# Kernel tuning notes

Measured on AMD Instinct MI355X. Metric: run time of the kernel, lower is better.

## Reference

```python
import jax, jax.numpy as jnp
import numpy as np

B, S, D, H = 16, 1024, 768, 12
HS = D // H  # head size = 64
NEG = -1000000.0  # module uses -1e6, not -inf


def setup_inputs() -> dict:
    key = jax.random.key(0)
    k1, k2, k3 = jax.random.split(key, 3)
    scale = 1.0 / np.sqrt(D)
    return {
        "x": jax.random.normal(k1, (B, S, D), dtype=jnp.float32),
        "W_qkv": jax.random.normal(k2, (D, 3 * D), dtype=jnp.float32) * scale,
        "b_qkv": jnp.zeros((3 * D,), dtype=jnp.float32),
        "W_o": jax.random.normal(k3, (D, D), dtype=jnp.float32) * scale,
        "b_o": jnp.zeros((D,), dtype=jnp.float32),
    }


def reference(x, W_qkv, b_qkv, W_o, b_o):
    qkv = x @ W_qkv + b_qkv                      # [B,S,3D]
    q, k, v = jnp.split(qkv, 3, axis=-1)         # each [B,S,D]
    q = q.reshape(B, S, H, HS)
    k = k.reshape(B, S, H, HS)
    v = v.reshape(B, S, H, HS)
    scores = jnp.einsum('bqhd,bkhd->bhqk', q, k) / np.sqrt(HS).astype(np.float32)
    causal = jnp.tril(jnp.ones((S, S), dtype=bool))
    scores = jnp.where(causal, scores, jnp.float32(NEG))
    probs = jax.nn.softmax(scores, axis=-1)      # dropout is eval-mode identity
    av = jnp.einsum('bhqk,bkhd->bqhd', probs, v).reshape(B, S, D)
    return av @ W_o + b_o
```

## Files before the change

### kernel.cpp

```cpp
#include <hip/hip_runtime.h>
#include <stdint.h>

typedef unsigned short u16;
typedef __attribute__((ext_vector_type(8))) short bf16x8;
typedef __attribute__((ext_vector_type(8))) u16 u16x8;
typedef __attribute__((ext_vector_type(4))) u16 u16x4;
typedef __attribute__((ext_vector_type(4))) float f32x4;
typedef __attribute__((ext_vector_type(16))) float f32x16;

#define B_ 16
#define S_ 1024
#define D_ 768
#define H_ 12

__device__ __forceinline__ float bf2f(u16 u) {
  unsigned int x = ((unsigned int)u) << 16;
  float f;
  __builtin_memcpy(&f, &x, 4);
  return f;
}
__device__ __forceinline__ u16 f2bf(float f) {
  unsigned int x;
  __builtin_memcpy(&x, &f, 4);
  x += 0x7fffu + ((x >> 16) & 1u);
  return (u16)(x >> 16);
}

#define MFMA16(a, b, c) __builtin_amdgcn_mfma_f32_16x16x32_bf16((a), (b), (c), 0, 0, 0)
#define MFMA32(a, b, c) __builtin_amdgcn_mfma_f32_32x32x16_bf16((a), (b), (c), 0, 0, 0)

#define GLD16(g, l)                                              \
  __builtin_amdgcn_global_load_lds(                              \
      (const __attribute__((address_space(1))) void*)(g),        \
      (__attribute__((address_space(3))) void*)(l), 16, 0, 0)

__global__ __launch_bounds__(256) void cvt_bf16(const float* __restrict__ in,
                                                u16* __restrict__ out, int n8) {
  const int i = blockIdx.x * 256 + threadIdx.x;
  if (i >= n8) return;
  const float4 a = *(const float4*)(in + (size_t)i * 8);
  const float4 b = *(const float4*)(in + (size_t)i * 8 + 4);
  u16x8 o;
  o[0] = f2bf(a.x); o[1] = f2bf(a.y); o[2] = f2bf(a.z); o[3] = f2bf(a.w);
  o[4] = f2bf(b.x); o[5] = f2bf(b.y); o[6] = f2bf(b.z); o[7] = f2bf(b.w);
  *(u16x8*)(out + (size_t)i * 8) = o;
}

__global__ __launch_bounds__(256) void transpose_cvt(const float* __restrict__ W,
                                                     u16* __restrict__ Wt, int K, int N) {
  __shared__ u16 t[32][33];
  const int n0 = blockIdx.x * 32, k0 = blockIdx.y * 32;
  const int tx = threadIdx.x & 31, ty = threadIdx.x >> 5;
#pragma unroll
  for (int i = 0; i < 32; i += 8)
    t[ty + i][tx] = f2bf(W[(size_t)(k0 + ty + i) * N + n0 + tx]);
  __syncthreads();
#pragma unroll
  for (int i = 0; i < 32; i += 8) Wt[(size_t)(n0 + ty + i) * K + k0 + tx] = t[tx][ty + i];
}

template <int MODE>
__global__ __launch_bounds__(256) void gemm_bt(const u16* __restrict__ A,
                                               const u16* __restrict__ Bt,
                                               const float* __restrict__ bias,
                                               u16* __restrict__ O0, u16* __restrict__ O1,
                                               u16* __restrict__ O2, float* __restrict__ Of,
                                               int M, int N, int K) {
  __shared__ u16 Al[128 * 32];
  __shared__ u16 Bl[128 * 32];
  const int tid = threadIdx.x;
  const int wid = tid >> 6, lane = tid & 63;
  const int lo = lane & 15, hi = lane >> 4;
  const int wr = wid >> 1, wc = wid & 1;
  const int m0 = blockIdx.x * 128, n0 = blockIdx.y * 128;
  const int rA = lane >> 2;
  const int kc = (lane & 3) * 8;
  f32x4 acc[4][4] = {};
  const int kiters = K >> 5;
  for (int kt = 0; kt < kiters; ++kt) {
    const int k0 = kt * 32;
    __syncthreads();
#pragma unroll
    for (int ld = 0; ld < 2; ++ld) {
      const int row = ld * 64 + wid * 16 + rA;
      const int boff = ld * 4096 + wid * 1024;
      GLD16(A + (size_t)(m0 + row) * K + k0 + kc, (char*)Al + boff);
      GLD16(Bt + (size_t)(n0 + row) * K + k0 + kc, (char*)Bl + boff);
    }
    __syncthreads();
    bf16x8 af[4], bfr[4];
#pragma unroll
    for (int i = 0; i < 4; ++i)
      af[i] = *(const bf16x8*)&Al[(wr * 64 + i * 16 + lo) * 32 + hi * 8];
#pragma unroll
    for (int j = 0; j < 4; ++j)
      bfr[j] = *(const bf16x8*)&Bl[(wc * 64 + j * 16 + lo) * 32 + hi * 8];
#pragma unroll
    for (int i = 0; i < 4; ++i)
#pragma unroll
      for (int j = 0; j < 4; ++j) acc[i][j] = MFMA16(af[i], bfr[j], acc[i][j]);
  }
#pragma unroll
  for (int j = 0; j < 4; ++j) {
    const int n = n0 + wc * 64 + j * 16 + lo;
    const float bv = bias[n];
#pragma unroll
    for (int i = 0; i < 4; ++i) {
#pragma unroll
      for (int r = 0; r < 4; ++r) {
        const int m = m0 + wr * 64 + i * 16 + hi * 4 + r;
        const float fv = acc[i][j][r] + bv;
        if (MODE == 0) {
          const u16 o = f2bf(fv);
          if (n0 < D_) {
            O0[(size_t)m * D_ + n] = o;
          } else if (n0 < 2 * D_) {
            O1[(size_t)m * D_ + (n - D_)] = o;
          } else {
            const int np = n - 2 * D_;
            O2[(((size_t)(m >> 10) * H_ + (np >> 6)) * 64 + (np & 63)) * S_ + (m & 1023)] = o;
          }
        } else {
          Of[(size_t)m * N + n] = fv;
        }
      }
    }
  }
}

__global__ __launch_bounds__(256) void attn_fwd2(const u16* __restrict__ Qb,
                                                 const u16* __restrict__ Kb,
                                                 const u16* __restrict__ VTb,
                                                 u16* __restrict__ att) {
  __shared__ u16 Kl[2048];
  __shared__ u16 Vl[2048];
  const int tid = threadIdx.x;
  const int lane = tid & 63, wid = tid >> 6;
  const int l31 = lane & 31, hi1 = lane >> 5;
  const int L = blockIdx.x + 8 * (blockIdx.y + 12 * blockIdx.z);
  const int bx = (L >> 3) & 7;
  const int P = (L & 7) + 8 * (L >> 6);
  const int h = P % 12, b = P / 12;
  const int q0 = bx * 128;
  const int qw0 = q0 + wid * 32;
  const int qg = qw0 + l31;
  const size_t rowbase = (size_t)b * S_;

  bf16x8 qf[4];
  {
    const u16* qp = Qb + (rowbase + qg) * D_ + h * 64 + hi1 * 8;
#pragma unroll
    for (int c = 0; c < 4; ++c) {
      bf16x8 v = *(const bf16x8*)(qp + c * 16);
#pragma unroll
      for (int j = 0; j < 8; ++j) v[j] = (short)f2bf(bf2f((u16)v[j]) * 0.125f);
      qf[c] = v;
    }
  }
  float mrun = -3.0e38f, lrun = 0.0f;
  f32x16 o0 = {}, o1 = {};

  const u16* kgp =
      Kb + (rowbase + (tid & 31)) * D_ + h * 64 + (tid >> 6) * 16 + ((tid >> 5) & 1) * 8;
  const u16* vgp = VTb +
                   (((size_t)b * H_ + h) * 64 + ((tid >> 6) & 1) * 32 + (tid & 31)) * S_ +
                   (tid >> 7) * 16 + ((tid >> 5) & 1) * 8;
  char* kdst = (char*)Kl + wid * 1024;
  char* vdst = (char*)Vl + wid * 1024;
  const char* kbase = (const char*)Kl + lane * 16;
  const char* vbase = (const char*)Vl + lane * 16;

  const int kvend = q0 + 128;
  for (int kv0 = 0; kv0 < kvend; kv0 += 32) {
    __syncthreads();
    GLD16(kgp + (size_t)kv0 * D_, kdst);
    GLD16(vgp + kv0, vdst);
    __syncthreads();
    if (kv0 > qw0 + 31) continue;

    f32x16 s = {};
#pragma unroll
    for (int c = 0; c < 4; ++c) s = MFMA32(*(const bf16x8*)(kbase + c * 1024), qf[c], s);

    if (kv0 + 31 > qw0) {
#pragma unroll
      for (int r = 0; r < 16; ++r) {
        const int kvg = kv0 + (r & 3) + 8 * (r >> 2) + 4 * hi1;
        if (kvg > qg) s[r] = -1.0e30f;
      }
    }
    float rm = s[0];
#pragma unroll
    for (int r = 1; r < 16; ++r) rm = fmaxf(rm, s[r]);
    rm = fmaxf(rm, __shfl_xor(rm, 32));
    const float mn = fmaxf(mrun, rm);
    const float fr = __expf(mrun - mn);
    mrun = mn;
    float p[16];
    float rs = 0.0f;
#pragma unroll
    for (int r = 0; r < 16; ++r) {
      p[r] = __expf(s[r] - mn);
      rs += p[r];
    }
    rs += __shfl_xor(rs, 32);
    lrun = lrun * fr + rs;
#pragma unroll
    for (int r = 0; r < 16; ++r) {
      o0[r] *= fr;
      o1[r] *= fr;
    }
    unsigned int pa[4], pb[4];
#pragma unroll
    for (int g = 0; g < 4; ++g) {
      pa[g] = (unsigned)f2bf(p[4 * g]) | ((unsigned)f2bf(p[4 * g + 1]) << 16);
      pb[g] = (unsigned)f2bf(p[4 * g + 2]) | ((unsigned)f2bf(p[4 * g + 3]) << 16);
    }
    const unsigned sa = __shfl_xor(hi1 ? pa[0] : pa[1], 32);
    const unsigned sb = __shfl_xor(hi1 ? pb[0] : pb[1], 32);
    const unsigned sc = __shfl_xor(hi1 ? pa[2] : pa[3], 32);
    const unsigned sd = __shfl_xor(hi1 ? pb[2] : pb[3], 32);
    const uint4 w0 = hi1 ? make_uint4(sa, sb, pa[1], pb[1]) : make_uint4(pa[0], pb[0], sa, sb);
    const uint4 w1 = hi1 ? make_uint4(sc, sd, pa[3], pb[3]) : make_uint4(pa[2], pb[2], sc, sd);
    bf16x8 pf0, pf1;
    __builtin_memcpy(&pf0, &w0, 16);
    __builtin_memcpy(&pf1, &w1, 16);
    o0 = MFMA32(*(const bf16x8*)(vbase + 0 * 1024), pf0, o0);
    o1 = MFMA32(*(const bf16x8*)(vbase + 1 * 1024), pf0, o1);
    o0 = MFMA32(*(const bf16x8*)(vbase + 2 * 1024), pf1, o0);
    o1 = MFMA32(*(const bf16x8*)(vbase + 3 * 1024), pf1, o1);
  }
  const float inv = 1.0f / lrun;
  u16* op = att + (rowbase + qg) * D_ + h * 64;
#pragma unroll
  for (int g = 0; g < 4; ++g) {
    u16x4 v0, v1;
#pragma unroll
    for (int j = 0; j < 4; ++j) {
      v0[j] = f2bf(o0[4 * g + j] * inv);
      v1[j] = f2bf(o1[4 * g + j] * inv);
    }
    *(u16x4*)(op + 8 * g + 4 * hi1) = v0;
    *(u16x4*)(op + 32 + 8 * g + 4 * hi1) = v1;
  }
}

extern "C" void kernel_launch(void* const* d_in, const int* in_sizes, int n_in, void* d_out,
                              int out_size, void* d_ws, size_t ws_size, hipStream_t stream) {
  const float *x = nullptr, *Wqkv = nullptr, *bqkv = nullptr, *Wo = nullptr, *bo = nullptr;
  for (int i = 0; i < n_in; ++i) {
    switch (in_sizes[i]) {
      case 16384 * 768:  x = (const float*)d_in[i]; break;
      case 768 * 2304:   Wqkv = (const float*)d_in[i]; break;
      case 2304:         bqkv = (const float*)d_in[i]; break;
      case 768 * 768:    Wo = (const float*)d_in[i]; break;
      case 768:          bo = (const float*)d_in[i]; break;
    }
  }
  float* out = (float*)d_out;

  char* ws = (char*)d_ws;
  u16* WqkvT = (u16*)(ws);
  u16* WoT = (u16*)(ws + 3538944);
  u16* Qb = (u16*)(ws + 4718592);
  u16* Kb = (u16*)(ws + 29884416);
  u16* VT = (u16*)(ws + 55050240);
  u16* xb = (u16*)d_out;
  u16* att = Qb;

  cvt_bf16<<<(16384 * 768 / 8 + 255) / 256, 256, 0, stream>>>(x, xb, 16384 * 768 / 8);
  transpose_cvt<<<dim3(2304 / 32, 768 / 32), 256, 0, stream>>>(Wqkv, WqkvT, 768, 2304);
  transpose_cvt<<<dim3(768 / 32, 768 / 32), 256, 0, stream>>>(Wo, WoT, 768, 768);
  gemm_bt<0><<<dim3(16384 / 128, 2304 / 128), 256, 0, stream>>>(
      xb, WqkvT, bqkv, Qb, Kb, VT, nullptr, 16384, 2304, 768);
  attn_fwd2<<<dim3(8, H_, B_), 256, 0, stream>>>(Qb, Kb, VT, att);
  gemm_bt<1><<<dim3(16384 / 128, 768 / 128), 256, 0, stream>>>(
      att, WoT, bo, nullptr, nullptr, nullptr, out, 16384, 768, 768);
}
```

Before: 257.4 us.

## Double-buffer GEMM shared-memory tiles to overlap global loads with MFMA

Doubles the LDS A/B tile buffers and prefetches the next K-slice directly into the alternate buffer, issued before the MFMAs on the current buffer. This replaces the two __syncthreads per iteration with a single vmcnt wait plus barrier, so global load latency can hide behind compute. It also raises wave priority around the MFMA block. The cost is doubled LDS per block, which may lower occupancy, and the wait is still a full vmcnt(0) at the end of each iteration.

```diff
diff --git a/kernel.cpp b/kernel.cpp
--- a/kernel.cpp
+++ b/kernel.cpp
@@ -66,8 +66,8 @@
                                                u16* __restrict__ O0, u16* __restrict__ O1,
                                                u16* __restrict__ O2, float* __restrict__ Of,
                                                int M, int N, int K) {
-  __shared__ u16 Al[128 * 32];
-  __shared__ u16 Bl[128 * 32];
+  __shared__ u16 Al[2 * 128 * 32];
+  __shared__ u16 Bl[2 * 128 * 32];
   const int tid = threadIdx.x;
   const int wid = tid >> 6, lane = tid & 63;
   const int lo = lane & 15, hi = lane >> 4;
@@ -75,30 +75,44 @@
   const int m0 = blockIdx.x * 128, n0 = blockIdx.y * 128;
   const int rA = lane >> 2;
   const int kc = (lane & 3) * 8;
+  const int srow = wid * 16 + rA;
   f32x4 acc[4][4] = {};
   const int kiters = K >> 5;
+
+  GLD16(A + (size_t)(m0 + srow) * K + kc, (char*)Al + wid * 1024);
+  GLD16(A + (size_t)(m0 + srow + 64) * K + kc, (char*)Al + 4096 + wid * 1024);
+  GLD16(Bt + (size_t)(n0 + srow) * K + kc, (char*)Bl + wid * 1024);
+  GLD16(Bt + (size_t)(n0 + srow + 64) * K + kc, (char*)Bl + 4096 + wid * 1024);
+  asm volatile("s_waitcnt vmcnt(0)" ::: "memory");
+  __builtin_amdgcn_s_barrier();
+
+  int cur = 0;
   for (int kt = 0; kt < kiters; ++kt) {
-    const int k0 = kt * 32;
-    __syncthreads();
-#pragma unroll
-    for (int ld = 0; ld < 2; ++ld) {
-      const int row = ld * 64 + wid * 16 + rA;
-      const int boff = ld * 4096 + wid * 1024;
-      GLD16(A + (size_t)(m0 + row) * K + k0 + kc, (char*)Al + boff);
-      GLD16(Bt + (size_t)(n0 + row) * K + k0 + kc, (char*)Bl + boff);
-    }
-    __syncthreads();
+    if (kt + 1 < kiters) {
+      const int k0 = (kt + 1) * 32;
+      const int nb = (cur ^ 1) * 8192;
+      GLD16(A + (size_t)(m0 + srow) * K + k0 + kc, (char*)Al + nb + wid * 1024);
+      GLD16(A + (size_t)(m0 + srow + 64) * K + k0 + kc, (char*)Al + nb + 4096 + wid * 1024);
+      GLD16(Bt + (size_t)(n0 + srow) * K + k0 + kc, (char*)Bl + nb + wid * 1024);
+      GLD16(Bt + (size_t)(n0 + srow + 64) * K + k0 + kc, (char*)Bl + nb + 4096 + wid * 1024);
+    }
+    const int cb = cur * 4096;
     bf16x8 af[4], bfr[4];
 #pragma unroll
     for (int i = 0; i < 4; ++i)
-      af[i] = *(const bf16x8*)&Al[(wr * 64 + i * 16 + lo) * 32 + hi * 8];
+      af[i] = *(const bf16x8*)&Al[cb + (wr * 64 + i * 16 + lo) * 32 + hi * 8];
 #pragma unroll
     for (int j = 0; j < 4; ++j)
-      bfr[j] = *(const bf16x8*)&Bl[(wc * 64 + j * 16 + lo) * 32 + hi * 8];
+      bfr[j] = *(const bf16x8*)&Bl[cb + (wc * 64 + j * 16 + lo) * 32 + hi * 8];
+    __builtin_amdgcn_s_setprio(1);
 #pragma unroll
     for (int i = 0; i < 4; ++i)
 #pragma unroll
       for (int j = 0; j < 4; ++j) acc[i][j] = MFMA16(af[i], bfr[j], acc[i][j]);
+    __builtin_amdgcn_s_setprio(0);
+    asm volatile("s_waitcnt vmcnt(0)" ::: "memory");
+    __builtin_amdgcn_s_barrier();
+    cur ^= 1;
   }
 #pragma unroll
   for (int j = 0; j < 4; ++j) {
```

New measurement: 251.9 us. -2.2%, faster.

## Replace GEMM with 256x256-tile double-buffered pipelined kernel and block swizzle

Applied to the files above, without the earlier changes.

Replaces the 128x128 single-buffered GEMM with a 512-thread kernel that computes 256x256 output tiles with K-step 64. LDS is double-buffered and global-to-LDS loads are interleaved between the quadrants of MFMA work, using explicit barriers, waitcnt and setprio. Block indices are swizzled so neighbouring workgroups share operand tiles in cache. The goal is to raise MFMA utilisation and data reuse for the QKV and output projections, at the cost of 128KB of LDS per block, more register pressure, and fewer blocks (192) for the output GEMM.

```diff
diff --git a/kernel.cpp b/kernel.cpp
--- a/kernel.cpp
+++ b/kernel.cpp
@@ -33,6 +33,9 @@
   __builtin_amdgcn_global_load_lds(                              \
       (const __attribute__((address_space(1))) void*)(g),        \
       (__attribute__((address_space(3))) void*)(l), 16, 0, 0)
+
+#define BAR() asm volatile("s_barrier" ::: "memory")
+#define LGKM0() asm volatile("s_waitcnt lgkmcnt(0)" ::: "memory")
 
 __global__ __launch_bounds__(256) void cvt_bf16(const float* __restrict__ in,
                                                 u16* __restrict__ out, int n8) {
@@ -60,56 +63,143 @@
 }
 
 template <int MODE>
-__global__ __launch_bounds__(256) void gemm_bt(const u16* __restrict__ A,
-                                               const u16* __restrict__ Bt,
-                                               const float* __restrict__ bias,
-                                               u16* __restrict__ O0, u16* __restrict__ O1,
-                                               u16* __restrict__ O2, float* __restrict__ Of,
-                                               int M, int N, int K) {
-  __shared__ u16 Al[128 * 32];
-  __shared__ u16 Bl[128 * 32];
+__global__ __launch_bounds__(512, 2) void gemm256(const u16* __restrict__ A,
+                                                  const u16* __restrict__ Bt,
+                                                  const float* __restrict__ bias,
+                                                  u16* __restrict__ O0, u16* __restrict__ O1,
+                                                  u16* __restrict__ O2, float* __restrict__ Of,
+                                                  int M, int N, int K) {
+  __shared__ u16 Ls[65536];
+  char* const ldsA = (char*)Ls;
+  char* const ldsB = (char*)Ls + 65536;
   const int tid = threadIdx.x;
   const int wid = tid >> 6, lane = tid & 63;
   const int lo = lane & 15, hi = lane >> 4;
-  const int wr = wid >> 1, wc = wid & 1;
-  const int m0 = blockIdx.x * 128, n0 = blockIdx.y * 128;
-  const int rA = lane >> 2;
-  const int kc = (lane & 3) * 8;
-  f32x4 acc[4][4] = {};
-  const int kiters = K >> 5;
-  for (int kt = 0; kt < kiters; ++kt) {
-    const int k0 = kt * 32;
-    __syncthreads();
-#pragma unroll
-    for (int ld = 0; ld < 2; ++ld) {
-      const int row = ld * 64 + wid * 16 + rA;
-      const int boff = ld * 4096 + wid * 1024;
-      GLD16(A + (size_t)(m0 + row) * K + k0 + kc, (char*)Al + boff);
-      GLD16(Bt + (size_t)(n0 + row) * K + k0 + kc, (char*)Bl + boff);
-    }
-    __syncthreads();
-    bf16x8 af[4], bfr[4];
-#pragma unroll
-    for (int i = 0; i < 4; ++i)
-      af[i] = *(const bf16x8*)&Al[(wr * 64 + i * 16 + lo) * 32 + hi * 8];
-#pragma unroll
-    for (int j = 0; j < 4; ++j)
-      bfr[j] = *(const bf16x8*)&Bl[(wc * 64 + j * 16 + lo) * 32 + hi * 8];
-#pragma unroll
-    for (int i = 0; i < 4; ++i)
-#pragma unroll
-      for (int j = 0; j < 4; ++j) acc[i][j] = MFMA16(af[i], bfr[j], acc[i][j]);
-  }
-#pragma unroll
-  for (int j = 0; j < 4; ++j) {
-    const int n = n0 + wc * 64 + j * 16 + lo;
+  const int wr = wid >> 2, wc = wid & 3;
+  const int nwg = gridDim.x;
+  const int swz = (blockIdx.x & 7) * (nwg >> 3) + (blockIdx.x >> 3);
+  const int nbm = M >> 8;
+  const int mb = swz % nbm, nb = swz / nbm;
+  const int m0 = mb * 256, n0 = nb * 256;
+
+  const u16* const srcA = A + (size_t)(m0 + lo) * K + hi * 8;
+  const u16* const srcB = Bt + (size_t)(n0 + lo) * K + hi * 8;
+  const size_t aoff = (size_t)(wid >> 1) * 16 * K + (wid & 1) * 32;
+
+#define STG_A(ha, kt, bb)                                                        \
+  do {                                                                           \
+    GLD16(srcA + (size_t)(ha) * 128 * K + aoff + (size_t)(kt) * 64,              \
+          ldsA + (bb) * 32768 + (ha) * 16384 + wid * 1024);                      \
+    GLD16(srcA + (size_t)(ha) * 128 * K + aoff + (size_t)64 * K + (size_t)(kt) * 64, \
+          ldsA + (bb) * 32768 + (ha) * 16384 + 8192 + wid * 1024);               \
+  } while (0)
+#define STG_B(hb, kt, bb)                                                        \
+  do {                                                                           \
+    GLD16(srcB + (size_t)(hb) * 128 * K + aoff + (size_t)(kt) * 64,              \
+          ldsB + (bb) * 32768 + (hb) * 16384 + wid * 1024);                      \
+    GLD16(srcB + (size_t)(hb) * 128 * K + aoff + (size_t)64 * K + (size_t)(kt) * 64, \
+          ldsB + (bb) * 32768 + (hb) * 16384 + 8192 + wid * 1024);               \
+  } while (0)
+
+  const char* const rdA = ldsA + wr * 16384 + lane * 16;
+  const char* const rdB = ldsB + (wc >> 1) * 16384 + (wc & 1) * 8192 + lane * 16;
+
+  f32x4 acc[8][4] = {};
+  const int T = K >> 6;
+
+  STG_A(0, 0, 0); STG_A(1, 0, 0); STG_B(0, 0, 0); STG_B(1, 0, 0);
+  STG_B(0, 1, 1); STG_A(0, 1, 1);
+  asm volatile("s_waitcnt vmcnt(4)" ::: "memory");
+  BAR();
+
+  for (int t = 0; t < T; ++t) {
+    const int curb = t & 1, nxtb = curb ^ 1;
+    const int cur = curb * 32768;
+    const bool s1 = (t + 1 < T), s2 = (t + 2 < T);
+    bf16x8 af[4][2], ah[4][2], bl[2][2], bh[2][2];
+#pragma unroll
+    for (int f = 0; f < 4; ++f)
+#pragma unroll
+      for (int s = 0; s < 2; ++s)
+        af[f][s] = *(const bf16x8*)(rdA + cur + (f * 2 + s) * 1024);
+#pragma unroll
+    for (int g = 0; g < 2; ++g)
+#pragma unroll
+      for (int s = 0; s < 2; ++s)
+        bl[g][s] = *(const bf16x8*)(rdB + cur + (g * 2 + s) * 1024);
+    if (s1) STG_A(1, t + 1, nxtb);
+    BAR(); LGKM0();
+    __builtin_amdgcn_s_setprio(1);
+#pragma unroll
+    for (int f = 0; f < 4; ++f)
+#pragma unroll
+      for (int g = 0; g < 2; ++g)
+#pragma unroll
+        for (int s = 0; s < 2; ++s) acc[f][g] = MFMA16(af[f][s], bl[g][s], acc[f][g]);
+    __builtin_amdgcn_s_setprio(0);
+    BAR();
+#pragma unroll
+    for (int g = 0; g < 2; ++g)
+#pragma unroll
+      for (int s = 0; s < 2; ++s)
+        bh[g][s] = *(const bf16x8*)(rdB + cur + ((2 + g) * 2 + s) * 1024);
+    if (s1) STG_B(1, t + 1, nxtb);
+    BAR(); LGKM0();
+    __builtin_amdgcn_s_setprio(1);
+#pragma unroll
+    for (int f = 0; f < 4; ++f)
+#pragma unroll
+      for (int g = 0; g < 2; ++g)
+#pragma unroll
+        for (int s = 0; s < 2; ++s) acc[f][2 + g] = MFMA16(af[f][s], bh[g][s], acc[f][2 + g]);
+    __builtin_amdgcn_s_setprio(0);
+    BAR();
+#pragma unroll
+    for (int f = 0; f < 4; ++f)
+#pragma unroll
+      for (int s = 0; s < 2; ++s)
+        ah[f][s] = *(const bf16x8*)(rdA + cur + ((4 + f) * 2 + s) * 1024);
+    if (s2) STG_B(0, t + 2, curb);
+    BAR(); LGKM0();
+    __builtin_amdgcn_s_setprio(1);
+#pragma unroll
+    for (int f = 0; f < 4; ++f)
+#pragma unroll
+      for (int g = 0; g < 2; ++g)
+#pragma unroll
+        for (int s = 0; s < 2; ++s)
+          acc[4 + f][2 + g] = MFMA16(ah[f][s], bh[g][s], acc[4 + f][2 + g]);
+    __builtin_amdgcn_s_setprio(0);
+    BAR();
+    if (s2) STG_A(0, t + 2, curb);
+    BAR();
+    __builtin_amdgcn_s_setprio(1);
+#pragma unroll
+    for (int f = 0; f < 4; ++f)
+#pragma unroll
+      for (int g = 0; g < 2; ++g)
+#pragma unroll
+        for (int s = 0; s < 2; ++s) acc[4 + f][g] = MFMA16(ah[f][s], bl[g][s], acc[4 + f][g]);
+    __builtin_amdgcn_s_setprio(0);
+    if (s2) {
+      asm volatile("s_waitcnt vmcnt(4)" ::: "memory");
+    } else if (s1) {
+      asm volatile("s_waitcnt vmcnt(0)" ::: "memory");
+    }
+    BAR();
+  }
+#undef STG_A
+#undef STG_B
+#pragma unroll
+  for (int g = 0; g < 4; ++g) {
+    const int n = n0 + wc * 64 + g * 16 + lo;
     const float bv = bias[n];
 #pragma unroll
-    for (int i = 0; i < 4; ++i) {
+    for (int f = 0; f < 8; ++f) {
 #pragma unroll
       for (int r = 0; r < 4; ++r) {
-        const int m = m0 + wr * 64 + i * 16 + hi * 4 + r;
-        const float fv = acc[i][j][r] + bv;
+        const int m = m0 + wr * 128 + f * 16 + hi * 4 + r;
+        const float fv = acc[f][g][r] + bv;
         if (MODE == 0) {
           const u16 o = f2bf(fv);
           if (n0 < D_) {
@@ -271,9 +361,7 @@
   cvt_bf16<<<(16384 * 768 / 8 + 255) / 256, 256, 0, stream>>>(x, xb, 16384 * 768 / 8);
   transpose_cvt<<<dim3(2304 / 32, 768 / 32), 256, 0, stream>>>(Wqkv, WqkvT, 768, 2304);
   transpose_cvt<<<dim3(768 / 32, 768 / 32), 256, 0, stream>>>(Wo, WoT, 768, 768);
-  gemm_bt<0><<<dim3(16384 / 128, 2304 / 128), 256, 0, stream>>>(
-      xb, WqkvT, bqkv, Qb, Kb, VT, nullptr, 16384, 2304, 768);
+  gemm256<0><<<576, 512, 0, stream>>>(xb, WqkvT, bqkv, Qb, Kb, VT, nullptr, 16384, 2304, 768);
   attn_fwd2<<<dim3(8, H_, B_), 256, 0, stream>>>(Qb, Kb, VT, att);
-  gemm_bt<1><<<dim3(16384 / 128, 768 / 128), 256, 0, stream>>>(
-      att, WoT, bo, nullptr, nullptr, nullptr, out, 16384, 768, 768);
-}
+  gemm256<1><<<192, 512, 0, stream>>>(att, WoT, bo, nullptr, nullptr, nullptr, out, 16384, 768, 768);
+}
```

Result: slower. 319.3 us (+24.0%).

## Pipeline GEMM with triple-buffered LDS, 128x256 tiles and swizzled block order

Applied to the files above, without the earlier changes.

Rewrites the bf16 GEMM so each block computes a 128x256 tile instead of 128x128. It prefetches two K-steps ahead into a three-stage LDS ring, using vmcnt waits and a single barrier per iteration. A 1D grid with an XCD-style swizzle maps blocks to tiles, and s_setprio raises priority around the MFMA burst. The goal is to hide global-load latency, halve the synchronisation per K-step and improve L2 reuse. The cost is more LDS and registers per block, and the fixed 256-column tile and swizzle assume shapes divisible by these sizes.

```diff
diff --git a/kernel.cpp b/kernel.cpp
--- a/kernel.cpp
+++ b/kernel.cpp
@@ -60,56 +60,84 @@
 }
 
 template <int MODE>
-__global__ __launch_bounds__(256) void gemm_bt(const u16* __restrict__ A,
-                                               const u16* __restrict__ Bt,
-                                               const float* __restrict__ bias,
-                                               u16* __restrict__ O0, u16* __restrict__ O1,
-                                               u16* __restrict__ O2, float* __restrict__ Of,
-                                               int M, int N, int K) {
-  __shared__ u16 Al[128 * 32];
-  __shared__ u16 Bl[128 * 32];
+__global__ __launch_bounds__(256, 2) void gemm_bt(const u16* __restrict__ A,
+                                                  const u16* __restrict__ Bt,
+                                                  const float* __restrict__ bias,
+                                                  u16* __restrict__ O0, u16* __restrict__ O1,
+                                                  u16* __restrict__ O2, float* __restrict__ Of,
+                                                  int M, int N, int K) {
+  __shared__ u16 Ls[36864];
+  char* const ldsA = (char*)Ls;
+  char* const ldsB = (char*)Ls + 24576;
   const int tid = threadIdx.x;
   const int wid = tid >> 6, lane = tid & 63;
   const int lo = lane & 15, hi = lane >> 4;
-  const int wr = wid >> 1, wc = wid & 1;
-  const int m0 = blockIdx.x * 128, n0 = blockIdx.y * 128;
-  const int rA = lane >> 2;
-  const int kc = (lane & 3) * 8;
-  f32x4 acc[4][4] = {};
-  const int kiters = K >> 5;
-  for (int kt = 0; kt < kiters; ++kt) {
-    const int k0 = kt * 32;
-    __syncthreads();
-#pragma unroll
-    for (int ld = 0; ld < 2; ++ld) {
-      const int row = ld * 64 + wid * 16 + rA;
-      const int boff = ld * 4096 + wid * 1024;
-      GLD16(A + (size_t)(m0 + row) * K + k0 + kc, (char*)Al + boff);
-      GLD16(Bt + (size_t)(n0 + row) * K + k0 + kc, (char*)Bl + boff);
-    }
-    __syncthreads();
-    bf16x8 af[4], bfr[4];
-#pragma unroll
-    for (int i = 0; i < 4; ++i)
-      af[i] = *(const bf16x8*)&Al[(wr * 64 + i * 16 + lo) * 32 + hi * 8];
-#pragma unroll
-    for (int j = 0; j < 4; ++j)
-      bfr[j] = *(const bf16x8*)&Bl[(wc * 64 + j * 16 + lo) * 32 + hi * 8];
-#pragma unroll
-    for (int i = 0; i < 4; ++i)
-#pragma unroll
-      for (int j = 0; j < 4; ++j) acc[i][j] = MFMA16(af[i], bfr[j], acc[i][j]);
-  }
-#pragma unroll
-  for (int j = 0; j < 4; ++j) {
-    const int n = n0 + wc * 64 + j * 16 + lo;
+  const int nwg = gridDim.x;
+  const int swz = (blockIdx.x & 7) * (nwg >> 3) + (blockIdx.x >> 3);
+  const int nbm = M >> 7;
+  const int mb = swz % nbm, nb = swz / nbm;
+  const int m0 = mb * 128, n0 = nb * 256;
+
+  const u16* const srcA = A + (size_t)(m0 + lo) * K + hi * 8;
+  const u16* const srcB = Bt + (size_t)(n0 + lo) * K + hi * 8;
+
+#define STAGE(kt, buf)                                                              \
+  do {                                                                              \
+    const size_t _k = (size_t)(kt) * 32;                                            \
+    GLD16(srcA + (size_t)(wid) * 16 * K + _k, ldsA + (buf) * 8192 + wid * 1024);    \
+    GLD16(srcA + (size_t)(wid + 4) * 16 * K + _k,                                   \
+          ldsA + (buf) * 8192 + (wid + 4) * 1024);                                  \
+    GLD16(srcB + (size_t)(wid) * 16 * K + _k, ldsB + (buf) * 16384 + wid * 1024);   \
+    GLD16(srcB + (size_t)(wid + 4) * 16 * K + _k,                                   \
+          ldsB + (buf) * 16384 + (wid + 4) * 1024);                                 \
+    GLD16(srcB + (size_t)(wid + 8) * 16 * K + _k,                                   \
+          ldsB + (buf) * 16384 + (wid + 8) * 1024);                                 \
+    GLD16(srcB + (size_t)(wid + 12) * 16 * K + _k,                                  \
+          ldsB + (buf) * 16384 + (wid + 12) * 1024);                                \
+  } while (0)
+
+  f32x4 acc[8][4] = {};
+  const int T = K >> 5;
+
+  STAGE(0, 0);
+  STAGE(1, 1);
+  asm volatile("s_waitcnt vmcnt(6)" ::: "memory");
+  __builtin_amdgcn_s_barrier();
+
+  for (int t = 0; t < T; ++t) {
+    if (t + 2 < T) STAGE(t + 2, (t + 2) % 3);
+    const int ab = (t % 3) * 8192, bb = (t % 3) * 16384;
+    bf16x8 af[8], bfr[4];
+#pragma unroll
+    for (int f = 0; f < 8; ++f)
+      af[f] = *(const bf16x8*)(ldsA + ab + f * 1024 + lane * 16);
+#pragma unroll
+    for (int g = 0; g < 4; ++g)
+      bfr[g] = *(const bf16x8*)(ldsB + bb + (wid * 4 + g) * 1024 + lane * 16);
+    __builtin_amdgcn_s_setprio(1);
+#pragma unroll
+    for (int f = 0; f < 8; ++f)
+#pragma unroll
+      for (int g = 0; g < 4; ++g) acc[f][g] = MFMA16(af[f], bfr[g], acc[f][g]);
+    __builtin_amdgcn_s_setprio(0);
+    if (t + 2 < T) {
+      asm volatile("s_waitcnt vmcnt(6)" ::: "memory");
+    } else if (t + 1 < T) {
+      asm volatile("s_waitcnt vmcnt(0)" ::: "memory");
+    }
+    __builtin_amdgcn_s_barrier();
+  }
+#undef STAGE
+#pragma unroll
+  for (int g = 0; g < 4; ++g) {
+    const int n = n0 + wid * 64 + g * 16 + lo;
     const float bv = bias[n];
 #pragma unroll
-    for (int i = 0; i < 4; ++i) {
+    for (int f = 0; f < 8; ++f) {
 #pragma unroll
       for (int r = 0; r < 4; ++r) {
-        const int m = m0 + wr * 64 + i * 16 + hi * 4 + r;
-        const float fv = acc[i][j][r] + bv;
+        const int m = m0 + f * 16 + hi * 4 + r;
+        const float fv = acc[f][g][r] + bv;
         if (MODE == 0) {
           const u16 o = f2bf(fv);
           if (n0 < D_) {
@@ -271,9 +299,9 @@
   cvt_bf16<<<(16384 * 768 / 8 + 255) / 256, 256, 0, stream>>>(x, xb, 16384 * 768 / 8);
   transpose_cvt<<<dim3(2304 / 32, 768 / 32), 256, 0, stream>>>(Wqkv, WqkvT, 768, 2304);
   transpose_cvt<<<dim3(768 / 32, 768 / 32), 256, 0, stream>>>(Wo, WoT, 768, 768);
-  gemm_bt<0><<<dim3(16384 / 128, 2304 / 128), 256, 0, stream>>>(
-      xb, WqkvT, bqkv, Qb, Kb, VT, nullptr, 16384, 2304, 768);
+  gemm_bt<0><<<128 * 9, 256, 0, stream>>>(xb, WqkvT, bqkv, Qb, Kb, VT, nullptr,
+                                          16384, 2304, 768);
   attn_fwd2<<<dim3(8, H_, B_), 256, 0, stream>>>(Qb, Kb, VT, att);
-  gemm_bt<1><<<dim3(16384 / 128, 768 / 128), 256, 0, stream>>>(
-      att, WoT, bo, nullptr, nullptr, nullptr, out, 16384, 768, 768);
-}
+  gemm_bt<1><<<128 * 3, 256, 0, stream>>>(att, WoT, bo, nullptr, nullptr, nullptr, out,
+                                          16384, 768, 768);
+}
```

New measurement: 318.0 us. 23.5% more time.
